# Performance work log

Hardware: AMD Instinct MI355X
Metric: run time of the kernel (lower is better)

## Reference

```python
import jax, jax.numpy as jnp
import numpy as np

N_NODES = 4096
HID = 64
N_STEP = 10
_OFFSETS = np.array([1, 2, 5, 11, 23, 47, 97, 193])  # circulant graph -> degree 16


def setup_inputs() -> dict:
    rng = np.random.default_rng(0)
    N = N_NODES
    i = np.repeat(np.arange(N), len(_OFFSETS))
    j = (i + np.tile(_OFFSETS, N)) % N
    vals = rng.normal(0.0, 0.5, i.shape).astype(np.float32)
    J = np.zeros((N, N), np.float32)
    J[i, j] = vals
    J[j, i] = vals  # symmetric coupling matrix
    row, col = np.nonzero(J)                      # E directed edges, row-major sorted
    key_fwd = row.astype(np.int64) * N + col
    rev = np.searchsorted(key_fwd, col.astype(np.int64) * N + row)  # reverse-edge index
    ru, cu = np.nonzero(np.triu(J))               # Eu upper-triangular edges
    u2e = np.searchsorted(key_fwd, ru.astype(np.int64) * N + cu)    # upper -> full edge index
    bias = rng.normal(0.0, 0.5, N).astype(np.float32)
    p = lambda *s: jnp.asarray(rng.normal(0.0, 0.1, s).astype(np.float32))
    return {
        'J': jnp.asarray(J), 'bias': jnp.asarray(bias),
        'gat_W': p(4, HID), 'gat_a': p(2 * HID, 1),
        'ci_W1': p(4, HID), 'ci_b1': jnp.zeros((HID,), jnp.float32),
        'ci_W2': p(HID, HID), 'ci_b2': jnp.zeros((HID,), jnp.float32),
        'ci_W3': p(HID, 1), 'ci_b3': jnp.zeros((1,), jnp.float32),
        'row': jnp.asarray(row.astype(np.int32)), 'col': jnp.asarray(col.astype(np.int32)),
        'rev': jnp.asarray(rev.astype(np.int32)),
        'ru': jnp.asarray(ru.astype(np.int32)), 'cu': jnp.asarray(cu.astype(np.int32)),
        'u2e': jnp.asarray(u2e.astype(np.int32)),
        'N_step': N_STEP, 'MPNNtype': 0,
    }


def reference(J, bias, gat_W, gat_a, ci_W1, ci_b1, ci_W2, ci_b2, ci_W3, ci_b3,
              row, col, rev, ru, cu, u2e, N_step, MPNNtype):
    N = J.shape[0]
    adj = (jnp.abs(J) > 0).astype(J.dtype)
    # node features: [-b, b, degree, row-sum of J]
    feat = jnp.stack([-bias, bias, adj.sum(1), J.sum(1)], axis=1)  # [N,4]
    # GAT scores: e[i,j] = leakyrelu([Wh_i || Wh_j] @ a) = leakyrelu(Wh_i@a1 + Wh_j@a2)
    Wh = feat @ gat_W                                  # [N,H]
    f1 = Wh @ gat_a[:HID, 0]
    f2 = Wh @ gat_a[HID:, 0]
    e = jax.nn.leaky_relu(f1[:, None] + f2[None, :], 0.2)
    att = jnp.where(adj > 0, jnp.exp(e), 0.0)
    Cij_matrix = 0.5 * (att + att.T)                   # [N,N]
    Cij_e = Cij_matrix[row, col]                       # [E]
    # Ci readout MLP
    h = jax.nn.relu(feat @ ci_W1 + ci_b1)
    h = jax.nn.relu(h @ ci_W2 + ci_b2)
    Ci = h @ ci_W3 + ci_b3                             # [N,1]
    dom = Ci + Cij_matrix.sum(1, keepdims=True)
    dom = jnp.sign(dom) * jnp.maximum(jnp.abs(dom), 0.1)  # clamp |.| >= 0.1
    bias_scale = bias / dom[:, 0]
    bx_scale = jnp.stack([-bias_scale, bias_scale], axis=1)  # [N,2]
    Jv = J[row, col]
    Jxy_scale = jnp.stack([jnp.stack([Jv, -Jv], -1),
                           jnp.stack([-Jv, Jv], -1)], axis=1) / Cij_e[:, None, None]  # [E,2,2]

    def node_update(em):
        # node_messages[j,:] = sum over edges (i->j) of em[e,:]
        nm = jax.ops.segment_sum(em, col, num_segments=N) / dom   # [N,2]
        lnZ = jnp.log(jnp.sum(jnp.exp(bx_scale + nm), axis=1, keepdims=True))
        return bx_scale + nm - lnZ, lnZ

    em0 = jnp.zeros((row.shape[0], 2), J.dtype)  # log of all-ones messages
    hidden0, lnZ0 = node_update(em0)

    def bp_step(carry, _):
        em, hidden, lnZ = carry
        ln_pj = hidden[row][:, :, None]     # [E,2,1]
        ln_zj = lnZ[row][:, :, None]        # [E,1,1]
        ln_mu_ij = em[rev][:, :, None]      # message on reverse edge, [E,2,1]
        M = jnp.exp(Jxy_scale + ln_pj + ln_zj - ln_mu_ij)          # [E,2,2]
        M = M / jnp.sum(jnp.max(M, axis=1), axis=1)[:, None, None]
        em_new = jnp.log(jnp.max(M ** Cij_e[:, None, None], axis=1))  # [E,2]
        hidden_new, lnZ_new = node_update(em_new)
        return (em_new, hidden_new, lnZ_new), None

    (em, hidden, lnZ), _ = jax.lax.scan(bp_step, (em0, hidden0, lnZ0), None, length=N_step)

    readout = jnp.exp(hidden)                           # [N,2]
    Js = J[ru, cu] / Cij_matrix[ru, cu]                 # [Eu]
    Jxy_u = jnp.exp(jnp.stack([jnp.stack([Js, -Js], -1),
                               jnp.stack([-Js, Js], -1)], axis=1))  # [Eu,2,2]
    temp_i = readout[cu] / jnp.exp(em[u2e])             # [Eu,2]
    temp_j = readout[ru] / jnp.exp(em[rev[u2e]])        # [Eu,2]
    pw = Jxy_u * temp_i[:, None, :] * temp_j[:, :, None]
    pw = pw / jnp.sum(pw, axis=(1, 2), keepdims=True)
    readout_pairwise = pw.reshape(-1, 4)                # [Eu,4]
    Cij_u = Cij_matrix[ru, cu]
    node_H = -jnp.sum(readout * jnp.log(readout + 1e-16), axis=1)
    edge_H = -jnp.sum(readout_pairwise * jnp.log(readout_pairwise + 1e-16), axis=1)
    node_entropy = Ci[:, 0] @ jax.lax.stop_gradient(node_H)
    edge_entropy = Cij_u @ jax.lax.stop_gradient(edge_H)
    return (readout, readout_pairwise, node_entropy + edge_entropy,
            node_entropy, edge_entropy, Ci[:, 0], Cij_u, dom)
```

## Files before the change

kernel.cpp:

```cpp
#include <hip/hip_runtime.h>
#include <cstddef>

#define TB    512
#define NB    128
#define NSTEP 10

__device__ __forceinline__ float lse2(float a, float b) {
    return fmaxf(a, b) + __logf(1.0f + __expf(-fabsf(a - b)));
}

__device__ __forceinline__ void stA(float2* p, float2 v) {
    union { float2 f; unsigned long long u; } x; x.f = v;
    __hip_atomic_store((unsigned long long*)p, x.u,
                       __ATOMIC_RELAXED, __HIP_MEMORY_SCOPE_AGENT);
}
__device__ __forceinline__ float2 ldA(const float2* p) {
    union { float2 f; unsigned long long u; } x;
    x.u = __hip_atomic_load((const unsigned long long*)p,
                            __ATOMIC_RELAXED, __HIP_MEMORY_SCOPE_AGENT);
    return x.f;
}

struct KParams {
    const float *J, *bias, *gat_W, *gat_a, *W1, *b1, *W2, *b2, *W3, *b3;
    const int *col, *rev, *ru, *cu, *u2e;
    int N, Eu;
    float2 *jsC, *fA, *uA, *uB, *emA, *emB;
    int*    bar;
    float  *ci_out, *dom_out, *ent;
    float2* ro_out;
    float4* rp_out;
    float*  cij_out;
};

__device__ __forceinline__ void grid_bar(int* flags, int expect) {
    __syncthreads();
    if (threadIdx.x == 0)
        __hip_atomic_store(&flags[blockIdx.x * 32], expect,
                           __ATOMIC_RELAXED, __HIP_MEMORY_SCOPE_AGENT);
    if (threadIdx.x < NB) {
        while (__hip_atomic_load(&flags[threadIdx.x * 32], __ATOMIC_RELAXED,
                                 __HIP_MEMORY_SCOPE_AGENT) < expect) {}
    }
    __syncthreads();
}

__global__ __launch_bounds__(TB) void k_fused(KParams p) {
    __shared__ float sW2[64 * 64];
    __shared__ float sh1[TB / 16][65];
    __shared__ float red[TB / 64];

    const int tidb = threadIdx.x;
    const int g = blockIdx.x * TB + tidb;
    const int i = g >> 4, t = g & 15;
    const int lane = tidb & 63;

    for (int k = tidb; k < 64 * 64; k += TB) sW2[k] = p.W2[k];
    if (g < 3) {
        __hip_atomic_store((int*)&p.ent[g], 0,
                           __ATOMIC_RELAXED, __HIP_MEMORY_SCOPE_AGENT);
    }
    stA(&p.emA[g], make_float2(0.0f, 0.0f));

    const int j  = p.col[g];
    const int rg = p.rev[g];
    const float Jv = p.J[(size_t)i * (size_t)p.N + (size_t)j];

    float rs = Jv;
    rs += __shfl_xor(rs, 1); rs += __shfl_xor(rs, 2);
    rs += __shfl_xor(rs, 4); rs += __shfl_xor(rs, 8);

    const float bi = p.bias[i];

    float s8 = 0.0f;
    if (lane < 8) {
        int k = lane & 3;
        const float* a = p.gat_a + ((lane < 4) ? 0 : 64);
        for (int h = 0; h < 64; ++h) s8 += p.gat_W[k * 64 + h] * a[h];
    }
    const float w10 = __shfl(s8, 0), w11 = __shfl(s8, 1), w12 = __shfl(s8, 2), w13 = __shfl(s8, 3);
    const float w20 = __shfl(s8, 4), w21 = __shfl(s8, 5), w22 = __shfl(s8, 6), w23 = __shfl(s8, 7);
    const float fd = 16.0f;
    const float f1i = -bi * w10 + bi * w11 + fd * w12 + rs * w13;
    const float f2i = -bi * w20 + bi * w21 + fd * w22 + rs * w23;

    const int nib = tidb >> 4;
    __syncthreads();
    #pragma unroll
    for (int m = 0; m < 4; ++m) {
        int h = t + 16 * m;
        float a = -bi * p.W1[h] + bi * p.W1[64 + h] + fd * p.W1[128 + h]
                + rs * p.W1[192 + h] + p.b1[h];
        sh1[nib][h] = fmaxf(a, 0.0f);
    }
    __syncthreads();
    float civ = 0.0f;
    #pragma unroll
    for (int m = 0; m < 4; ++m) {
        int o = t + 16 * m;
        float acc = p.b2[o];
        for (int h = 0; h < 64; ++h) acc += sh1[nib][h] * sW2[h * 64 + o];
        civ += fmaxf(acc, 0.0f) * p.W3[o];
    }
    civ += __shfl_xor(civ, 1); civ += __shfl_xor(civ, 2);
    civ += __shfl_xor(civ, 4); civ += __shfl_xor(civ, 8);
    const float ci = civ + p.b3[0];

    if (t == 0) {
        stA(&p.fA[i], make_float2(f1i, f2i));
        p.ci_out[i] = ci;
    }
    grid_bar(p.bar, 1);

    const float2 fj = ldA(&p.fA[j]);
    float x1 = f1i + fj.y; x1 = (x1 > 0.0f) ? x1 : 0.2f * x1;
    float x2 = fj.x + f2i; x2 = (x2 > 0.0f) ? x2 : 0.2f * x2;
    const float C  = 0.5f * (__expf(x1) + __expf(x2));
    const float js = Jv / C;
    stA(&p.jsC[g], make_float2(js, C));

    float sc = C;
    sc += __shfl_xor(sc, 1); sc += __shfl_xor(sc, 2);
    sc += __shfl_xor(sc, 4); sc += __shfl_xor(sc, 8);
    const float s  = ci + sc;
    const float cl = fmaxf(fabsf(s), 0.1f);
    const float d  = (s > 0.0f) ? cl : ((s < 0.0f) ? -cl : 0.0f);
    const float rd = 1.0f / d;
    const float bs = bi * rd;
    if (t == 0) {
        p.dom_out[i] = d;
        stA(&p.uA[i], make_float2(-bs, bs));
    }
    grid_bar(p.bar, 2);

    int eE = 0, eR = 0, eC = 0, eEr = 0;
    float jse = 0.0f, Ce = 0.0f;
    if (g < p.Eu) {
        eE = p.u2e[g]; eR = p.ru[g]; eC = p.cu[g];
        eEr = p.rev[eE];
        const float2 jc = ldA(&p.jsC[eE]);
        jse = jc.x; Ce = jc.y;
    }

    float2 *uP = p.uA, *uQ = p.uB, *emP = p.emA, *emQ = p.emB;
    for (int st = 0; st < NSTEP; ++st) {
        const float2 uj = ldA(&uP[j]);
        const float2 mu = ldA(&emP[rg]);
        const float a0 = uj.x - mu.x, a1 = uj.y - mu.y;
        const float t0 = fmaxf( js + a0, -js + a1);
        const float t1 = fmaxf(-js + a0,  js + a1);
        const float ls = lse2(t0, t1);
        const float e0 = C * (t0 - ls), e1 = C * (t1 - ls);
        stA(&emQ[g], make_float2(e0, e1));

        float nm0 = e0, nm1 = e1;
        nm0 += __shfl_xor(nm0, 1); nm1 += __shfl_xor(nm1, 1);
        nm0 += __shfl_xor(nm0, 2); nm1 += __shfl_xor(nm1, 2);
        nm0 += __shfl_xor(nm0, 4); nm1 += __shfl_xor(nm1, 4);
        nm0 += __shfl_xor(nm0, 8); nm1 += __shfl_xor(nm1, 8);
        const float v0 = -bs + nm0 * rd, v1 = bs + nm1 * rd;
        if (t == 0) stA(&uQ[i], make_float2(v0, v1));

        if (st == NSTEP - 1) {
            float nodeC = 0.0f;
            if (t == 0) {
                const float lz = lse2(v0, v1);
                const float r0 = __expf(v0 - lz), r1 = __expf(v1 - lz);
                p.ro_out[i] = make_float2(r0, r1);
                const float H = -(r0 * __logf(r0 + 1e-16f) + r1 * __logf(r1 + 1e-16f));
                nodeC = ci * H;
            }
            for (int off = 32; off > 0; off >>= 1) nodeC += __shfl_down(nodeC, off);
            const int wv = tidb >> 6;
            if (lane == 0) red[wv] = nodeC;
            __syncthreads();
            if (tidb == 0) {
                float sn = 0.0f;
                #pragma unroll
                for (int w = 0; w < TB / 64; ++w) sn += red[w];
                atomicAdd(&p.ent[0], sn);
                atomicAdd(&p.ent[1], sn);
            }
        }
        grid_bar(p.bar, 3 + st);
        float2* tp;
        tp = uP;  uP  = uQ;  uQ  = tp;
        tp = emP; emP = emQ; emQ = tp;
    }

    float edgeC = 0.0f;
    if (g < p.Eu) {
        const float2 uc = ldA(&uP[eC]), ur = ldA(&uP[eR]);
        const float lc = lse2(uc.x, uc.y);
        const float lr = lse2(ur.x, ur.y);
        const float2 eme = ldA(&emP[eEr]);
        const float2 emr = ldA(&emP[eE]);
        const float ti0 = (uc.x - lc) - eme.x, ti1 = (uc.y - lc) - eme.y;
        const float tj0 = (ur.x - lr) - emr.x, tj1 = (ur.y - lr) - emr.y;
        const float L00 =  jse + ti0 + tj0;
        const float L01 = -jse + ti1 + tj0;
        const float L10 = -jse + ti0 + tj1;
        const float L11 =  jse + ti1 + tj1;
        const float mL = fmaxf(fmaxf(L00, L01), fmaxf(L10, L11));
        float p00 = __expf(L00 - mL), p01 = __expf(L01 - mL);
        float p10 = __expf(L10 - mL), p11 = __expf(L11 - mL);
        const float inv = 1.0f / (p00 + p01 + p10 + p11);
        p00 *= inv; p01 *= inv; p10 *= inv; p11 *= inv;
        p.rp_out[g] = make_float4(p00, p01, p10, p11);
        p.cij_out[g] = Ce;
        const float H = -(p00 * __logf(p00 + 1e-16f) + p01 * __logf(p01 + 1e-16f)
                        + p10 * __logf(p10 + 1e-16f) + p11 * __logf(p11 + 1e-16f));
        edgeC = Ce * H;
    }
    for (int off = 32; off > 0; off >>= 1) edgeC += __shfl_down(edgeC, off);
    const int wv = tidb >> 6;
    if (lane == 0) red[wv] = edgeC;
    __syncthreads();
    if (tidb == 0) {
        float se = 0.0f;
        #pragma unroll
        for (int w = 0; w < TB / 64; ++w) se += red[w];
        atomicAdd(&p.ent[0], se);
        atomicAdd(&p.ent[2], se);
    }
}

extern "C" void kernel_launch(void* const* d_in, const int* in_sizes, int n_in,
                              void* d_out, int out_size, void* d_ws, size_t ws_size,
                              hipStream_t stream) {
    const int N  = in_sizes[1];
    const int E  = in_sizes[10];
    const int Eu = in_sizes[13];

    float* out = (float*)d_out;
    size_t OFF_RP  = 2 * (size_t)N;
    size_t OFF_ENT = OFF_RP + 4 * (size_t)Eu;

    char* w = (char*)d_ws;
    auto carve = [&](size_t bytes) {
        void* q = (void*)w;
        w += (bytes + 255) & ~(size_t)255;
        return q;
    };

    KParams p;
    p.J     = (const float*)d_in[0];
    p.bias  = (const float*)d_in[1];
    p.gat_W = (const float*)d_in[2];
    p.gat_a = (const float*)d_in[3];
    p.W1    = (const float*)d_in[4];
    p.b1    = (const float*)d_in[5];
    p.W2    = (const float*)d_in[6];
    p.b2    = (const float*)d_in[7];
    p.W3    = (const float*)d_in[8];
    p.b3    = (const float*)d_in[9];
    p.col   = (const int*)d_in[11];
    p.rev   = (const int*)d_in[12];
    p.ru    = (const int*)d_in[13];
    p.cu    = (const int*)d_in[14];
    p.u2e   = (const int*)d_in[15];
    p.N = N; p.Eu = Eu;

    p.jsC   = (float2*)carve((size_t)E * 8);
    p.fA    = (float2*)carve((size_t)N * 8);
    p.uA    = (float2*)carve((size_t)N * 8);
    p.uB    = (float2*)carve((size_t)N * 8);
    p.emA   = (float2*)carve((size_t)E * 8);
    p.emB   = (float2*)carve((size_t)E * 8);
    p.bar   = (int*)carve((size_t)NB * 128);

    p.ro_out  = (float2*)out;
    p.rp_out  = (float4*)(out + OFF_RP);
    p.ent     = out + OFF_ENT;
    p.ci_out  = p.ent + 3;
    p.cij_out = p.ci_out + N;
    p.dom_out = p.cij_out + Eu;

    hipMemsetAsync(p.bar, 0, (size_t)NB * 128, stream);
    k_fused<<<dim3(NB), dim3(TB), 0, stream>>>(p);
}
```

Before: 163.0 us.

## Recompute neighbor features locally and track reverse messages in registers

After: 160.4 us. No clear change (-1.6%).

```diff
diff --git a/kernel.cpp b/kernel.cpp
--- a/kernel.cpp
+++ b/kernel.cpp
@@ -25,7 +25,7 @@
     const float *J, *bias, *gat_W, *gat_a, *W1, *b1, *W2, *b2, *W3, *b3;
     const int *col, *rev, *ru, *cu, *u2e;
     int N, Eu;
-    float2 *jsC, *fA, *uA, *uB, *emA, *emB;
+    float2 *jsC, *uA, *uB, *em;
     int*    bar;
     float  *ci_out, *dom_out, *ent;
     float2* ro_out;
@@ -60,17 +60,23 @@
         __hip_atomic_store((int*)&p.ent[g], 0,
                            __ATOMIC_RELAXED, __HIP_MEMORY_SCOPE_AGENT);
     }
-    stA(&p.emA[g], make_float2(0.0f, 0.0f));
 
     const int j  = p.col[g];
-    const int rg = p.rev[g];
     const float Jv = p.J[(size_t)i * (size_t)p.N + (size_t)j];
 
     float rs = Jv;
     rs += __shfl_xor(rs, 1); rs += __shfl_xor(rs, 2);
     rs += __shfl_xor(rs, 4); rs += __shfl_xor(rs, 8);
 
-    const float bi = p.bias[i];
+    float rsj = 0.0f;
+    {
+        const int* colj = p.col + 16 * j;
+        const float* Jrow = p.J + (size_t)j * (size_t)p.N;
+        #pragma unroll 4
+        for (int tt = 0; tt < 16; ++tt) rsj += Jrow[colj[tt]];
+    }
+
+    const float bi = p.bias[i], bj = p.bias[j];
 
     float s8 = 0.0f;
     if (lane < 8) {
@@ -81,8 +87,20 @@
     const float w10 = __shfl(s8, 0), w11 = __shfl(s8, 1), w12 = __shfl(s8, 2), w13 = __shfl(s8, 3);
     const float w20 = __shfl(s8, 4), w21 = __shfl(s8, 5), w22 = __shfl(s8, 6), w23 = __shfl(s8, 7);
     const float fd = 16.0f;
-    const float f1i = -bi * w10 + bi * w11 + fd * w12 + rs * w13;
-    const float f2i = -bi * w20 + bi * w21 + fd * w22 + rs * w23;
+    const float f1i = -bi * w10 + bi * w11 + fd * w12 + rs  * w13;
+    const float f2i = -bi * w20 + bi * w21 + fd * w22 + rs  * w23;
+    const float f1j = -bj * w10 + bj * w11 + fd * w12 + rsj * w13;
+    const float f2j = -bj * w20 + bj * w21 + fd * w22 + rsj * w23;
+
+    float x1 = f1i + f2j; x1 = (x1 > 0.0f) ? x1 : 0.2f * x1;
+    float x2 = f1j + f2i; x2 = (x2 > 0.0f) ? x2 : 0.2f * x2;
+    const float C  = 0.5f * (__expf(x1) + __expf(x2));
+    const float js = Jv / C;
+    stA(&p.jsC[g], make_float2(js, C));
+
+    float sc = C;
+    sc += __shfl_xor(sc, 1); sc += __shfl_xor(sc, 2);
+    sc += __shfl_xor(sc, 4); sc += __shfl_xor(sc, 8);
 
     const int nib = tidb >> 4;
     __syncthreads();
@@ -106,32 +124,17 @@
     civ += __shfl_xor(civ, 4); civ += __shfl_xor(civ, 8);
     const float ci = civ + p.b3[0];
 
-    if (t == 0) {
-        stA(&p.fA[i], make_float2(f1i, f2i));
-        p.ci_out[i] = ci;
-    }
-    grid_bar(p.bar, 1);
-
-    const float2 fj = ldA(&p.fA[j]);
-    float x1 = f1i + fj.y; x1 = (x1 > 0.0f) ? x1 : 0.2f * x1;
-    float x2 = fj.x + f2i; x2 = (x2 > 0.0f) ? x2 : 0.2f * x2;
-    const float C  = 0.5f * (__expf(x1) + __expf(x2));
-    const float js = Jv / C;
-    stA(&p.jsC[g], make_float2(js, C));
-
-    float sc = C;
-    sc += __shfl_xor(sc, 1); sc += __shfl_xor(sc, 2);
-    sc += __shfl_xor(sc, 4); sc += __shfl_xor(sc, 8);
     const float s  = ci + sc;
     const float cl = fmaxf(fabsf(s), 0.1f);
     const float d  = (s > 0.0f) ? cl : ((s < 0.0f) ? -cl : 0.0f);
     const float rd = 1.0f / d;
     const float bs = bi * rd;
     if (t == 0) {
+        p.ci_out[i] = ci;
         p.dom_out[i] = d;
         stA(&p.uA[i], make_float2(-bs, bs));
     }
-    grid_bar(p.bar, 2);
+    grid_bar(p.bar, 1);
 
     int eE = 0, eR = 0, eC = 0, eEr = 0;
     float jse = 0.0f, Ce = 0.0f;
@@ -142,30 +145,38 @@
         jse = jc.x; Ce = jc.y;
     }
 
-    float2 *uP = p.uA, *uQ = p.uB, *emP = p.emA, *emQ = p.emB;
+    float in0 = 0.0f, in1 = 0.0f;
+    float out0 = 0.0f, out1 = 0.0f;
+    float ui0 = -bs, ui1 = bs;
+    float2 *uP = p.uA, *uQ = p.uB;
     for (int st = 0; st < NSTEP; ++st) {
         const float2 uj = ldA(&uP[j]);
-        const float2 mu = ldA(&emP[rg]);
-        const float a0 = uj.x - mu.x, a1 = uj.y - mu.y;
+        const float a0 = uj.x - out0, a1 = uj.y - out1;
         const float t0 = fmaxf( js + a0, -js + a1);
         const float t1 = fmaxf(-js + a0,  js + a1);
         const float ls = lse2(t0, t1);
-        const float e0 = C * (t0 - ls), e1 = C * (t1 - ls);
-        stA(&emQ[g], make_float2(e0, e1));
-
-        float nm0 = e0, nm1 = e1;
+        const float ni0 = C * (t0 - ls), ni1 = C * (t1 - ls);
+        const float b0 = ui0 - in0, b1 = ui1 - in1;
+        const float q0 = fmaxf( js + b0, -js + b1);
+        const float q1 = fmaxf(-js + b0,  js + b1);
+        const float qs = lse2(q0, q1);
+        out0 = C * (q0 - qs); out1 = C * (q1 - qs);
+        in0 = ni0; in1 = ni1;
+
+        float nm0 = in0, nm1 = in1;
         nm0 += __shfl_xor(nm0, 1); nm1 += __shfl_xor(nm1, 1);
         nm0 += __shfl_xor(nm0, 2); nm1 += __shfl_xor(nm1, 2);
         nm0 += __shfl_xor(nm0, 4); nm1 += __shfl_xor(nm1, 4);
         nm0 += __shfl_xor(nm0, 8); nm1 += __shfl_xor(nm1, 8);
-        const float v0 = -bs + nm0 * rd, v1 = bs + nm1 * rd;
-        if (t == 0) stA(&uQ[i], make_float2(v0, v1));
+        ui0 = -bs + nm0 * rd; ui1 = bs + nm1 * rd;
+        if (t == 0) stA(&uQ[i], make_float2(ui0, ui1));
 
         if (st == NSTEP - 1) {
+            stA(&p.em[g], make_float2(in0, in1));
             float nodeC = 0.0f;
             if (t == 0) {
-                const float lz = lse2(v0, v1);
-                const float r0 = __expf(v0 - lz), r1 = __expf(v1 - lz);
+                const float lz = lse2(ui0, ui1);
+                const float r0 = __expf(ui0 - lz), r1 = __expf(ui1 - lz);
                 p.ro_out[i] = make_float2(r0, r1);
                 const float H = -(r0 * __logf(r0 + 1e-16f) + r1 * __logf(r1 + 1e-16f));
                 nodeC = ci * H;
@@ -182,10 +193,8 @@
                 atomicAdd(&p.ent[1], sn);
             }
         }
-        grid_bar(p.bar, 3 + st);
-        float2* tp;
-        tp = uP;  uP  = uQ;  uQ  = tp;
-        tp = emP; emP = emQ; emQ = tp;
+        grid_bar(p.bar, 2 + st);
+        float2* tp = uP; uP = uQ; uQ = tp;
     }
 
     float edgeC = 0.0f;
@@ -193,8 +202,8 @@
         const float2 uc = ldA(&uP[eC]), ur = ldA(&uP[eR]);
         const float lc = lse2(uc.x, uc.y);
         const float lr = lse2(ur.x, ur.y);
-        const float2 eme = ldA(&emP[eEr]);
-        const float2 emr = ldA(&emP[eE]);
+        const float2 eme = ldA(&p.em[eEr]);
+        const float2 emr = ldA(&p.em[eE]);
         const float ti0 = (uc.x - lc) - eme.x, ti1 = (uc.y - lc) - eme.y;
         const float tj0 = (ur.x - lr) - emr.x, tj1 = (ur.y - lr) - emr.y;
         const float L00 =  jse + ti0 + tj0;
@@ -262,11 +271,9 @@
     p.N = N; p.Eu = Eu;
 
     p.jsC   = (float2*)carve((size_t)E * 8);
-    p.fA    = (float2*)carve((size_t)N * 8);
     p.uA    = (float2*)carve((size_t)N * 8);
     p.uB    = (float2*)carve((size_t)N * 8);
-    p.emA   = (float2*)carve((size_t)E * 8);
-    p.emB   = (float2*)carve((size_t)E * 8);
+    p.em    = (float2*)carve((size_t)E * 8);
     p.bar   = (int*)carve((size_t)NB * 128);
 
     p.ro_out  = (float2*)out;
```
